# Kernel optimization log

Hardware: AMD Instinct MI355X
Metric: run time of the kernel (lower is better)

## Reference

```python
import jax, jax.numpy as jnp
import numpy as np

H = 2048          # hidden_size
I = 1024          # moe_intermediate_size
E = 32            # n_routed_experts
K = 4             # num_experts_per_tok
N_SHARED = 1
EPS = 1e-6


def setup_inputs() -> dict:
    key = jax.random.key(0)
    ks = jax.random.split(key, 8)
    s = 1.0 / np.sqrt(H)
    si = 1.0 / np.sqrt(I)
    return {
        "hidden_states": jax.random.normal(ks[0], (1, 4096, H), jnp.float32),
        "norm_w": jnp.ones((H,), jnp.float32),
        "gate_w": jax.random.normal(ks[1], (E, H), jnp.float32) * s,      # MoEGate.weight
        "w13": jax.random.normal(ks[2], (E, H, 2 * I), jnp.float32) * s,  # fused w1w3
        "w2": jax.random.normal(ks[3], (E, I, H), jnp.float32) * si,      # fused w2
        "shared_gate_w": jax.random.normal(ks[4], (H, I * N_SHARED), jnp.float32) * s,
        "shared_up_w": jax.random.normal(ks[5], (H, I * N_SHARED), jnp.float32) * s,
        "shared_down_w": jax.random.normal(ks[6], (I * N_SHARED, H), jnp.float32) * si,
    }


def _rmsnorm(x, w, eps=EPS):
    var = jnp.mean(jnp.square(x), axis=-1, keepdims=True)
    return x * jax.lax.rsqrt(var + eps) * w


def _moe_core(x, gate_w, w13, w2):
    # x: [T, H] (post-norm tokens)
    T = x.shape[0]
    N = T * K
    C = 2 * N // E

    # --- gate (fp32, F.linear) ---
    logits = jnp.einsum("th,eh->te", x.astype(jnp.float32), gate_w.astype(jnp.float32))
    scores = jax.nn.softmax(logits, axis=-1)
    topk_w, topk_ids = jax.lax.top_k(scores, K)           # [T, K]
    topk_w = topk_w / jnp.sum(topk_w, axis=-1, keepdims=True)  # norm_topk_prob

    # --- dispatch: sort token-expert pairs by expert ---
    flat_ids = topk_ids.reshape(-1)                        # [N] int
    flat_w = topk_w.reshape(-1)                            # [N]
    order = jnp.argsort(flat_ids)                          # stable sort by expert
    sorted_eid = flat_ids[order]                           # [N]
    tok = order // K                                       # source token per sorted slot
    counts = jnp.zeros((E,), jnp.int32).at[flat_ids].add(1)  # tokens_per_expert
    starts = jnp.cumsum(counts) - counts
    pos = jnp.arange(N) - starts[sorted_eid]               # position within expert group

    # scatter tokens into [E, C, H] buffer (OOB rows dropped; C sized so this ~never happens)
    buf = jnp.zeros((E, C, x.shape[1]), x.dtype).at[sorted_eid, pos].set(x[tok], mode="drop")

    # --- grouped expert FFN (swiglu) ---
    gu = jnp.einsum("ech,ehf->ecf", buf, w13)              # [E, C, 2I]
    g, u = jnp.split(gu, 2, axis=-1)
    act = jax.nn.silu(g) * u                               # swiglu
    eo = jnp.einsum("eci,eih->ech", act, w2)               # [E, C, H]

    # --- combine: gather back and weighted scatter-add per source token ---
    out_slots = eo[sorted_eid, pos]                        # [N, H]
    routed = jnp.zeros_like(x).at[tok].add(out_slots * flat_w[order][:, None])
    return routed


def reference(hidden_states, norm_w, gate_w, w13, w2, shared_gate_w, shared_up_w, shared_down_w):
    B, S, Hd = hidden_states.shape
    residual = hidden_states
    h = _rmsnorm(hidden_states, norm_w)                    # post_attention_layernorm
    x = h.reshape(-1, Hd)                                  # [T, H]

    routed = _moe_core(x, gate_w, w13, w2)                 # routed experts output

    # shared experts MLP (swiglu)
    shared = (jax.nn.silu(x @ shared_gate_w) * (x @ shared_up_w)) @ shared_down_w

    out = residual + (routed + shared).reshape(B, S, Hd)
    return out
```

## Files before the change

### kernel.cpp

```cpp
#include <hip/hip_runtime.h>
#include <hip/hip_bf16.h>
#include <math.h>

#define HD 2048
#define ID 1024
#define NE 32
#define TOPK 4
#define NTOK 4096
#define NSLOT (NTOK*TOPK)

typedef __attribute__((ext_vector_type(4))) float f32x4;
typedef __attribute__((ext_vector_type(8))) short bf16x8;
typedef unsigned short u16;
typedef unsigned int u32;

union U32x4BF { uint4 u; bf16x8 h; };

static __device__ __forceinline__ u16 f2bf(float f) {
  union { float f; u32 u; } v; v.f = f;
  u32 r = v.u + 0x7fffu + ((v.u >> 16) & 1u);
  return (u16)(r >> 16);
}

static __device__ __forceinline__ u32 cvtpk(float lo, float hi) {
  u32 r;
  asm("v_cvt_pk_bf16_f32 %0, %1, %2" : "=v"(r) : "v"(lo), "v"(hi));
  return r;
}

static __device__ __forceinline__ void barrier_lgkm() {
  asm volatile("s_waitcnt lgkmcnt(0)" ::: "memory");
  __builtin_amdgcn_s_barrier();
}

static __device__ __forceinline__ void loadBreg(const float* __restrict__ bg,
                                                const float* __restrict__ bu,
                                                u32 o0, u32 o1, u32 o2, u32 o3,
                                                u32 ldb, float bs[4][8]) {
  #pragma unroll
  for (int j = 0; j < 8; ++j) {
    bs[0][j] = bg[o0 + j*ldb];
    bs[1][j] = bu[o1 + j*ldb];
    bs[2][j] = bg[o2 + j*ldb];
    bs[3][j] = bu[o3 + j*ldb];
  }
}

static __device__ __forceinline__ void cvtB(const float bs[4][8], bf16x8 bfr[4]) {
  #pragma unroll
  for (int fn = 0; fn < 4; ++fn) {
    U32x4BF ub;
    ub.u.x = cvtpk(bs[fn][0], bs[fn][1]);
    ub.u.y = cvtpk(bs[fn][2], bs[fn][3]);
    ub.u.z = cvtpk(bs[fn][4], bs[fn][5]);
    ub.u.w = cvtpk(bs[fn][6], bs[fn][7]);
    bfr[fn] = ub.h;
  }
}

__global__ __launch_bounds__(256) void k_rmsnorm(const float* __restrict__ x,
                                                 const float* __restrict__ w,
                                                 u16* __restrict__ xn,
                                                 float* __restrict__ out) {
  int t = blockIdx.x, tid = threadIdx.x;
  const float* row = x + (size_t)t * HD;
  float4 v0 = ((const float4*)row)[tid*2+0];
  float4 v1 = ((const float4*)row)[tid*2+1];
  float* orow = out + (size_t)t * HD;
  ((float4*)orow)[tid*2+0] = v0;
  ((float4*)orow)[tid*2+1] = v1;
  float ss = v0.x*v0.x+v0.y*v0.y+v0.z*v0.z+v0.w*v0.w
           + v1.x*v1.x+v1.y*v1.y+v1.z*v1.z+v1.w*v1.w;
  #pragma unroll
  for (int d=1; d<64; d<<=1) ss += __shfl_xor(ss, d);
  __shared__ float red[4];
  if ((tid&63)==0) red[tid>>6] = ss;
  __syncthreads();
  float rs = rsqrtf((red[0]+red[1]+red[2]+red[3]) * (1.0f/HD) + 1e-6f);
  const float* wp = w + tid*8;
  float a[8] = {v0.x,v0.y,v0.z,v0.w,v1.x,v1.y,v1.z,v1.w};
  uint4 o;
  o.x = (u32)f2bf(a[0]*rs*wp[0]) | ((u32)f2bf(a[1]*rs*wp[1])<<16);
  o.y = (u32)f2bf(a[2]*rs*wp[2]) | ((u32)f2bf(a[3]*rs*wp[3])<<16);
  o.z = (u32)f2bf(a[4]*rs*wp[4]) | ((u32)f2bf(a[5]*rs*wp[5])<<16);
  o.w = (u32)f2bf(a[6]*rs*wp[6]) | ((u32)f2bf(a[7]*rs*wp[7])<<16);
  ((uint4*)xn)[(size_t)t*(HD/8) + tid] = o;
}

__global__ __launch_bounds__(256) void k_gate(const float* __restrict__ x,
                                              const float* __restrict__ w,
                                              const float* __restrict__ gw,
                                              int* __restrict__ topk_id,
                                              float* __restrict__ topk_w,
                                              int* __restrict__ counts) {
  __shared__ float xs[HD];
  __shared__ float red[4];
  __shared__ float logits[NE];
  int t = blockIdx.x, tid = threadIdx.x;
  const float* row = x + (size_t)t*HD;
  float4 v0 = ((const float4*)row)[tid*2+0];
  float4 v1 = ((const float4*)row)[tid*2+1];
  float ss = v0.x*v0.x+v0.y*v0.y+v0.z*v0.z+v0.w*v0.w
           + v1.x*v1.x+v1.y*v1.y+v1.z*v1.z+v1.w*v1.w;
  #pragma unroll
  for (int d=1; d<64; d<<=1) ss += __shfl_xor(ss, d);
  if ((tid&63)==0) red[tid>>6] = ss;
  __syncthreads();
  float rs = 1.0f / sqrtf((red[0]+red[1]+red[2]+red[3]) * (1.0f/HD) + 1e-6f);
  const float* wp = w + tid*8;
  float a[8] = {v0.x,v0.y,v0.z,v0.w,v1.x,v1.y,v1.z,v1.w};
  #pragma unroll
  for (int j=0;j<8;++j) xs[tid*8+j] = a[j]*rs*wp[j];
  __syncthreads();
  int wave = tid>>6, lane = tid&63;
  for (int ei=0; ei<8; ++ei) {
    int e = wave*8 + ei;
    const float* g = gw + (size_t)e*HD;
    float s = 0.f;
    #pragma unroll
    for (int j=0;j<HD/64;++j) s += xs[lane + j*64] * g[lane + j*64];
    #pragma unroll
    for (int d=1; d<64; d<<=1) s += __shfl_xor(s, d);
    if (lane==0) logits[e] = s;
  }
  __syncthreads();
  if (tid==0) {
    float best[TOPK]; int bid[TOPK]; unsigned used = 0;
    for (int k2=0;k2<TOPK;++k2) {
      float bv = -1e30f; int bi = 0;
      for (int i2=0;i2<NE;++i2)
        if (!((used>>i2)&1u) && logits[i2] > bv) { bv = logits[i2]; bi = i2; }
      used |= 1u<<bi; best[k2] = bv; bid[k2] = bi;
    }
    float mx = best[0], sum = 0.f, wv[TOPK];
    for (int k2=0;k2<TOPK;++k2) { wv[k2] = expf(best[k2]-mx); sum += wv[k2]; }
    float inv = 1.f/sum;
    for (int k2=0;k2<TOPK;++k2) {
      topk_id[t*TOPK+k2] = bid[k2];
      topk_w[t*TOPK+k2] = wv[k2]*inv;
      atomicAdd(&counts[bid[k2]], 1);
    }
  }
}

__global__ void k_zero(int* counts, int* cursors) {
  int i = threadIdx.x;
  if (i < NE) { counts[i] = 0; cursors[i] = 0; }
}

__global__ void k_scan(const int* __restrict__ counts, int* __restrict__ starts) {
  if (threadIdx.x==0 && blockIdx.x==0) {
    int acc = 0;
    for (int e=0;e<NE;++e) { starts[e] = acc; acc += counts[e]; }
  }
}

__global__ __launch_bounds__(256) void k_dispatch(const int* __restrict__ topk_id,
                                                  const float* __restrict__ topk_w,
                                                  const int* __restrict__ starts,
                                                  int* __restrict__ cursors,
                                                  int* __restrict__ slot_tok,
                                                  float* __restrict__ slot_w) {
  int i = blockIdx.x*256 + threadIdx.x;
  int e = topk_id[i];
  int p = atomicAdd(&cursors[e], 1);
  int slot = starts[e] + p;
  slot_tok[slot] = i >> 2;
  slot_w[slot] = topk_w[i];
}

__global__ __launch_bounds__(256, 2) void k_gemm_up(
    const u16* __restrict__ A, const float* __restrict__ w13,
    const float* __restrict__ sgw, const float* __restrict__ suw,
    const int* __restrict__ counts, const int* __restrict__ starts,
    const int* __restrict__ slot_tok,
    u16* __restrict__ act, u16* __restrict__ sact) {
  __shared__ u16 Al[2][4096];
  __shared__ int rowL[128];
  int t = threadIdx.x;
  int n0 = blockIdx.x * 128;
  int m0 = blockIdx.y * 128;
  int e  = blockIdx.z;
  bool routed = (e < NE);
  int M, rowbase;
  u16* actOut;
  if (routed) { M = counts[e]; rowbase = starts[e]; actOut = act; if (m0 >= M) return; }
  else { M = NTOK; rowbase = 0; actOut = sact; }
  if (t < 128) {
    int m = m0 + t;
    rowL[t] = routed ? slot_tok[rowbase + (m < M ? m : M-1)] : m;
  }
  __syncthreads();
  int r0i = t>>2;
  int segA = ((t&3) ^ ((r0i>>1)&3)) << 3;
  const u16* srcA0 = A + (size_t)rowL[r0i]*HD + segA;
  const u16* srcA1 = A + (size_t)rowL[r0i+64]*HD + segA;

  int lane = t&63, wn = t>>6;
  int l15 = lane&15, l4 = lane>>4;
  int aoffb = l15*32 + ((l4 ^ ((l15>>1)&3))<<3);

  const float *bbg, *bbu;
  u32 ldb, o0, o1, o2, o3;
  {
    int c0 = n0 + (wn*2+0)*16 + l15;
    int c1 = n0 + (wn*2+1)*16 + l15;
    if (routed) {
      ldb = 2*ID;
      bbg = w13 + (size_t)e*HD*2*ID; bbu = bbg;
      u32 rb = (u32)(l4*8)*ldb;
      o0 = rb + c0; o1 = rb + c0 + ID; o2 = rb + c1; o3 = rb + c1 + ID;
    } else {
      ldb = ID;
      bbg = sgw; bbu = suw;
      u32 rb = (u32)(l4*8)*ldb;
      o0 = rb + c0; o1 = rb + c0; o2 = rb + c1; o3 = rb + c1;
    }
  }
  u32 kadv = 32*ldb;

  f32x4 acc[8][4];
  #pragma unroll
  for (int fm=0;fm<8;++fm)
    #pragma unroll
    for (int fn=0;fn<4;++fn)
      acc[fm][fn] = (f32x4){0.f,0.f,0.f,0.f};

  uint4 aA0 = *(const uint4*)srcA0, aA1 = *(const uint4*)srcA1;
  srcA0 += 32; srcA1 += 32;
  float bsA[4][8]; loadBreg(bbg, bbu, o0,o1,o2,o3, ldb, bsA);
  o0 += kadv; o1 += kadv; o2 += kadv; o3 += kadv;
  uint4 aB0 = *(const uint4*)srcA0, aB1 = *(const uint4*)srcA1;
  srcA0 += 32; srcA1 += 32;
  float bsB[4][8]; loadBreg(bbg, bbu, o0,o1,o2,o3, ldb, bsB);
  o0 += kadv; o1 += kadv; o2 += kadv; o3 += kadv;
  *(uint4*)&Al[0][t*8] = aA0;
  *(uint4*)&Al[0][2048 + t*8] = aA1;
  barrier_lgkm();

  const int kiter = HD/32;
  for (int kt = 0; kt < kiter; kt += 2) {
    {
      bool pf = (kt+2 < kiter);
      if (pf) { aA0 = *(const uint4*)srcA0; aA1 = *(const uint4*)srcA1; srcA0 += 32; srcA1 += 32; }
      bf16x8 bfr[4]; cvtB(bsA, bfr);
      if (pf) { loadBreg(bbg, bbu, o0,o1,o2,o3, ldb, bsA);
                o0 += kadv; o1 += kadv; o2 += kadv; o3 += kadv; }
      __builtin_amdgcn_s_setprio(1);
      #pragma unroll
      for (int fm=0; fm<8; ++fm) {
        bf16x8 af = *(const bf16x8*)&Al[0][aoffb + fm*512];
        #pragma unroll
        for (int fn=0; fn<4; ++fn)
          acc[fm][fn] = __builtin_amdgcn_mfma_f32_16x16x32_bf16(af, bfr[fn], acc[fm][fn], 0,0,0);
      }
      __builtin_amdgcn_s_setprio(0);
      *(uint4*)&Al[1][t*8] = aB0;
      *(uint4*)&Al[1][2048 + t*8] = aB1;
      barrier_lgkm();
    }
    {
      bool pf = (kt+3 < kiter);
      if (pf) { aB0 = *(const uint4*)srcA0; aB1 = *(const uint4*)srcA1; srcA0 += 32; srcA1 += 32; }
      bf16x8 bfr[4]; cvtB(bsB, bfr);
      if (pf) { loadBreg(bbg, bbu, o0,o1,o2,o3, ldb, bsB);
                o0 += kadv; o1 += kadv; o2 += kadv; o3 += kadv; }
      __builtin_amdgcn_s_setprio(1);
      #pragma unroll
      for (int fm=0; fm<8; ++fm) {
        bf16x8 af = *(const bf16x8*)&Al[1][aoffb + fm*512];
        #pragma unroll
        for (int fn=0; fn<4; ++fn)
          acc[fm][fn] = __builtin_amdgcn_mfma_f32_16x16x32_bf16(af, bfr[fn], acc[fm][fn], 0,0,0);
      }
      __builtin_amdgcn_s_setprio(0);
      if (kt+2 < kiter) {
        *(uint4*)&Al[0][t*8] = aA0;
        *(uint4*)&Al[0][2048 + t*8] = aA1;
      }
      barrier_lgkm();
    }
  }
  #pragma unroll
  for (int fm=0; fm<8; ++fm) {
    #pragma unroll
    for (int fq=0; fq<2; ++fq) {
      f32x4 g = acc[fm][2*fq], u = acc[fm][2*fq+1];
      int col = n0 + (wn*2+fq)*16 + l15;
      #pragma unroll
      for (int r=0;r<4;++r) {
        int mloc = fm*16 + l4*4 + r;
        int m = m0 + mloc;
        if (m < M) {
          float gv = g[r];
          float av = gv / (1.f + expf(-gv)) * u[r];
          actOut[(size_t)(rowbase+m)*ID + col] = f2bf(av);
        }
      }
    }
  }
}

__global__ __launch_bounds__(256, 2) void k_gemm_down(
    const u16* __restrict__ act, const u16* __restrict__ sact,
    const float* __restrict__ w2, const float* __restrict__ sdw,
    const int* __restrict__ counts, const int* __restrict__ starts,
    const int* __restrict__ slot_tok, const float* __restrict__ slot_w,
    float* __restrict__ out) {
  __shared__ u16 Al[2][4096];
  __shared__ int tokL[128];
  __shared__ float wL[128];
  int t = threadIdx.x;
  int n0 = blockIdx.x * 256;
  int m0 = blockIdx.y * 128;
  int e  = blockIdx.z;
  bool routed = (e < NE);
  int M, rowbase;
  const u16* A;
  if (routed) { M = counts[e]; rowbase = starts[e]; A = act; if (m0 >= M) return; }
  else { M = NTOK; rowbase = 0; A = sact; }
  if (routed && t < 128) {
    int m = m0 + t;
    tokL[t] = (m<M) ? slot_tok[rowbase+m] : 0;
    wL[t]   = (m<M) ? slot_w[rowbase+m]  : 0.f;
  }
  if (routed) __syncthreads();
  int r0i = t>>2;
  int segA = ((t&3) ^ ((r0i>>1)&3)) << 3;
  int am0 = m0 + r0i, am1 = m0 + r0i + 64;
  const u16* srcA0 = A + (size_t)(rowbase + (am0 < M ? am0 : M-1))*ID + segA;
  const u16* srcA1 = A + (size_t)(rowbase + (am1 < M ? am1 : M-1))*ID + segA;

  int lane = t&63, wn = t>>6;
  int l15 = lane&15, l4 = lane>>4;
  int aoffb = l15*32 + ((l4 ^ ((l15>>1)&3))<<3);

  const float* bb = routed ? (w2 + (size_t)e*ID*HD) : sdw;
  const u32 ldb = HD;
  u32 rb = (u32)(l4*8)*ldb;
  u32 o0 = rb + n0 + wn*64 + 0*16 + l15;
  u32 o1 = rb + n0 + wn*64 + 1*16 + l15;
  u32 o2 = rb + n0 + wn*64 + 2*16 + l15;
  u32 o3 = rb + n0 + wn*64 + 3*16 + l15;
  const u32 kadv = 32*ldb;

  f32x4 acc[8][4];
  #pragma unroll
  for (int fm=0;fm<8;++fm)
    #pragma unroll
    for (int fn=0;fn<4;++fn)
      acc[fm][fn] = (f32x4){0.f,0.f,0.f,0.f};

  uint4 aA0 = *(const uint4*)srcA0, aA1 = *(const uint4*)srcA1;
  srcA0 += 32; srcA1 += 32;
  float bsA[4][8]; loadBreg(bb, bb, o0,o1,o2,o3, ldb, bsA);
  o0 += kadv; o1 += kadv; o2 += kadv; o3 += kadv;
  uint4 aB0 = *(const uint4*)srcA0, aB1 = *(const uint4*)srcA1;
  srcA0 += 32; srcA1 += 32;
  float bsB[4][8]; loadBreg(bb, bb, o0,o1,o2,o3, ldb, bsB);
  o0 += kadv; o1 += kadv; o2 += kadv; o3 += kadv;
  *(uint4*)&Al[0][t*8] = aA0;
  *(uint4*)&Al[0][2048 + t*8] = aA1;
  barrier_lgkm();

  const int kiter = ID/32;
  for (int kt = 0; kt < kiter; kt += 2) {
    {
      bool pf = (kt+2 < kiter);
      if (pf) { aA0 = *(const uint4*)srcA0; aA1 = *(const uint4*)srcA1; srcA0 += 32; srcA1 += 32; }
      bf16x8 bfr[4]; cvtB(bsA, bfr);
      if (pf) { loadBreg(bb, bb, o0,o1,o2,o3, ldb, bsA);
                o0 += kadv; o1 += kadv; o2 += kadv; o3 += kadv; }
      __builtin_amdgcn_s_setprio(1);
      #pragma unroll
      for (int fm=0; fm<8; ++fm) {
        bf16x8 af = *(const bf16x8*)&Al[0][aoffb + fm*512];
        #pragma unroll
        for (int fn=0; fn<4; ++fn)
          acc[fm][fn] = __builtin_amdgcn_mfma_f32_16x16x32_bf16(af, bfr[fn], acc[fm][fn], 0,0,0);
      }
      __builtin_amdgcn_s_setprio(0);
      *(uint4*)&Al[1][t*8] = aB0;
      *(uint4*)&Al[1][2048 + t*8] = aB1;
      barrier_lgkm();
    }
    {
      bool pf = (kt+3 < kiter);
      if (pf) { aB0 = *(const uint4*)srcA0; aB1 = *(const uint4*)srcA1; srcA0 += 32; srcA1 += 32; }
      bf16x8 bfr[4]; cvtB(bsB, bfr);
      if (pf) { loadBreg(bb, bb, o0,o1,o2,o3, ldb, bsB);
                o0 += kadv; o1 += kadv; o2 += kadv; o3 += kadv; }
      __builtin_amdgcn_s_setprio(1);
      #pragma unroll
      for (int fm=0; fm<8; ++fm) {
        bf16x8 af = *(const bf16x8*)&Al[1][aoffb + fm*512];
        #pragma unroll
        for (int fn=0; fn<4; ++fn)
          acc[fm][fn] = __builtin_amdgcn_mfma_f32_16x16x32_bf16(af, bfr[fn], acc[fm][fn], 0,0,0);
      }
      __builtin_amdgcn_s_setprio(0);
      if (kt+2 < kiter) {
        *(uint4*)&Al[0][t*8] = aA0;
        *(uint4*)&Al[0][2048 + t*8] = aA1;
      }
      barrier_lgkm();
    }
  }
  #pragma unroll
  for (int fm=0; fm<8; ++fm) {
    #pragma unroll
    for (int fn=0; fn<4; ++fn) {
      f32x4 v = acc[fm][fn];
      int col = n0 + wn*64 + fn*16 + l15;
      #pragma unroll
      for (int r=0;r<4;++r) {
        int mloc = fm*16 + l4*4 + r;
        int m = m0 + mloc;
        if (m < M) {
          if (routed) {
            atomicAdd(&out[(size_t)tokL[mloc]*HD + col], v[r]*wL[mloc]);
          } else {
            atomicAdd(&out[(size_t)m*HD + col], v[r]);
          }
        }
      }
    }
  }
}

extern "C" void kernel_launch(void* const* d_in, const int* in_sizes, int n_in,
                              void* d_out, int out_size, void* d_ws, size_t ws_size,
                              hipStream_t stream) {
  const float* x    = (const float*)d_in[0];
  const float* nw   = (const float*)d_in[1];
  const float* gw   = (const float*)d_in[2];
  const float* w13  = (const float*)d_in[3];
  const float* w2   = (const float*)d_in[4];
  const float* sgw  = (const float*)d_in[5];
  const float* suw  = (const float*)d_in[6];
  const float* sdw  = (const float*)d_in[7];
  float* out = (float*)d_out;

  char* p = (char*)d_ws;
  u16* xn   = (u16*)p;  p += (size_t)NTOK*HD*2;
  u16* act  = (u16*)p;  p += (size_t)NSLOT*ID*2;
  u16* sact = (u16*)p;  p += (size_t)NTOK*ID*2;
  int*   topk_id  = (int*)p;   p += (size_t)NTOK*TOPK*4;
  float* topk_w   = (float*)p; p += (size_t)NTOK*TOPK*4;
  int*   slot_tok = (int*)p;   p += (size_t)NSLOT*4;
  float* slot_w   = (float*)p; p += (size_t)NSLOT*4;
  int*   counts   = (int*)p;   p += 64*4;
  int*   cursors  = (int*)p;   p += 64*4;
  int*   starts   = (int*)p;   p += 64*4;

  k_zero<<<1, 64, 0, stream>>>(counts, cursors);
  k_rmsnorm<<<NTOK, 256, 0, stream>>>(x, nw, xn, out);
  k_gate<<<NTOK, 256, 0, stream>>>(x, nw, gw, topk_id, topk_w, counts);
  k_scan<<<1, 1, 0, stream>>>(counts, starts);
  k_dispatch<<<NSLOT/256, 256, 0, stream>>>(topk_id, topk_w, starts, cursors, slot_tok, slot_w);

  k_gemm_up<<<dim3(ID/128, 32, NE+1), 256, 0, stream>>>(
      xn, w13, sgw, suw, counts, starts, slot_tok, act, sact);
  k_gemm_down<<<dim3(HD/256, 32, NE+1), 256, 0, stream>>>(
      act, sact, w2, sdw, counts, starts, slot_tok, slot_w, out);
}
```

Before: 752.9 us.

## Fuse rmsnorm into gate kernel and retile GEMMs to 2x2 wave grid

Merges the rmsnorm and gate kernels into one prep kernel, so the input rows are read once and one launch goes away. Both grouped GEMMs move from a 1x4 wave layout to a 2x2 layout with half the N tile per block. This halves the per-wave accumulators, which allows the occupancy hint to rise from 2 to 3 blocks. The cost is that each block reloads the fp32 weight tiles over twice as many blocks, adding redundant global traffic and bf16 conversion work.

New measurement: 1.239 ms. 1.65x slower.

```diff
diff --git a/kernel.cpp b/kernel.cpp
--- a/kernel.cpp
+++ b/kernel.cpp
@@ -35,14 +35,14 @@
 
 static __device__ __forceinline__ void loadBreg(const float* __restrict__ bg,
                                                 const float* __restrict__ bu,
-                                                u32 o0, u32 o1, u32 o2, u32 o3,
-                                                u32 ldb, float bs[4][8]) {
+                                                const u32 o[4], u32 ldb,
+                                                float bs[4][8]) {
   #pragma unroll
   for (int j = 0; j < 8; ++j) {
-    bs[0][j] = bg[o0 + j*ldb];
-    bs[1][j] = bu[o1 + j*ldb];
-    bs[2][j] = bg[o2 + j*ldb];
-    bs[3][j] = bu[o3 + j*ldb];
+    bs[0][j] = bg[o[0] + j*ldb];
+    bs[1][j] = bu[o[1] + j*ldb];
+    bs[2][j] = bg[o[2] + j*ldb];
+    bs[3][j] = bu[o[3] + j*ldb];
   }
 }
 
@@ -58,38 +58,11 @@
   }
 }
 
-__global__ __launch_bounds__(256) void k_rmsnorm(const float* __restrict__ x,
-                                                 const float* __restrict__ w,
-                                                 u16* __restrict__ xn,
-                                                 float* __restrict__ out) {
-  int t = blockIdx.x, tid = threadIdx.x;
-  const float* row = x + (size_t)t * HD;
-  float4 v0 = ((const float4*)row)[tid*2+0];
-  float4 v1 = ((const float4*)row)[tid*2+1];
-  float* orow = out + (size_t)t * HD;
-  ((float4*)orow)[tid*2+0] = v0;
-  ((float4*)orow)[tid*2+1] = v1;
-  float ss = v0.x*v0.x+v0.y*v0.y+v0.z*v0.z+v0.w*v0.w
-           + v1.x*v1.x+v1.y*v1.y+v1.z*v1.z+v1.w*v1.w;
-  #pragma unroll
-  for (int d=1; d<64; d<<=1) ss += __shfl_xor(ss, d);
-  __shared__ float red[4];
-  if ((tid&63)==0) red[tid>>6] = ss;
-  __syncthreads();
-  float rs = rsqrtf((red[0]+red[1]+red[2]+red[3]) * (1.0f/HD) + 1e-6f);
-  const float* wp = w + tid*8;
-  float a[8] = {v0.x,v0.y,v0.z,v0.w,v1.x,v1.y,v1.z,v1.w};
-  uint4 o;
-  o.x = (u32)f2bf(a[0]*rs*wp[0]) | ((u32)f2bf(a[1]*rs*wp[1])<<16);
-  o.y = (u32)f2bf(a[2]*rs*wp[2]) | ((u32)f2bf(a[3]*rs*wp[3])<<16);
-  o.z = (u32)f2bf(a[4]*rs*wp[4]) | ((u32)f2bf(a[5]*rs*wp[5])<<16);
-  o.w = (u32)f2bf(a[6]*rs*wp[6]) | ((u32)f2bf(a[7]*rs*wp[7])<<16);
-  ((uint4*)xn)[(size_t)t*(HD/8) + tid] = o;
-}
-
-__global__ __launch_bounds__(256) void k_gate(const float* __restrict__ x,
+__global__ __launch_bounds__(256) void k_prep(const float* __restrict__ x,
                                               const float* __restrict__ w,
                                               const float* __restrict__ gw,
+                                              u16* __restrict__ xn,
+                                              float* __restrict__ out,
                                               int* __restrict__ topk_id,
                                               float* __restrict__ topk_w,
                                               int* __restrict__ counts) {
@@ -100,17 +73,27 @@
   const float* row = x + (size_t)t*HD;
   float4 v0 = ((const float4*)row)[tid*2+0];
   float4 v1 = ((const float4*)row)[tid*2+1];
+  float* orow = out + (size_t)t * HD;
+  ((float4*)orow)[tid*2+0] = v0;
+  ((float4*)orow)[tid*2+1] = v1;
   float ss = v0.x*v0.x+v0.y*v0.y+v0.z*v0.z+v0.w*v0.w
            + v1.x*v1.x+v1.y*v1.y+v1.z*v1.z+v1.w*v1.w;
   #pragma unroll
   for (int d=1; d<64; d<<=1) ss += __shfl_xor(ss, d);
   if ((tid&63)==0) red[tid>>6] = ss;
   __syncthreads();
-  float rs = 1.0f / sqrtf((red[0]+red[1]+red[2]+red[3]) * (1.0f/HD) + 1e-6f);
+  float rs = rsqrtf((red[0]+red[1]+red[2]+red[3]) * (1.0f/HD) + 1e-6f);
   const float* wp = w + tid*8;
   float a[8] = {v0.x,v0.y,v0.z,v0.w,v1.x,v1.y,v1.z,v1.w};
-  #pragma unroll
-  for (int j=0;j<8;++j) xs[tid*8+j] = a[j]*rs*wp[j];
+  float nv[8];
+  #pragma unroll
+  for (int j=0;j<8;++j) { nv[j] = a[j]*rs*wp[j]; xs[tid*8+j] = nv[j]; }
+  uint4 o;
+  o.x = (u32)f2bf(nv[0]) | ((u32)f2bf(nv[1])<<16);
+  o.y = (u32)f2bf(nv[2]) | ((u32)f2bf(nv[3])<<16);
+  o.z = (u32)f2bf(nv[4]) | ((u32)f2bf(nv[5])<<16);
+  o.w = (u32)f2bf(nv[6]) | ((u32)f2bf(nv[7])<<16);
+  ((uint4*)xn)[(size_t)t*(HD/8) + tid] = o;
   __syncthreads();
   int wave = tid>>6, lane = tid&63;
   for (int ei=0; ei<8; ++ei) {
@@ -169,7 +152,7 @@
   slot_w[slot] = topk_w[i];
 }
 
-__global__ __launch_bounds__(256, 2) void k_gemm_up(
+__global__ __launch_bounds__(256, 3) void k_gemm_up(
     const u16* __restrict__ A, const float* __restrict__ w13,
     const float* __restrict__ sgw, const float* __restrict__ suw,
     const int* __restrict__ counts, const int* __restrict__ starts,
@@ -178,7 +161,7 @@
   __shared__ u16 Al[2][4096];
   __shared__ int rowL[128];
   int t = threadIdx.x;
-  int n0 = blockIdx.x * 128;
+  int n0 = blockIdx.x * 64;
   int m0 = blockIdx.y * 128;
   int e  = blockIdx.z;
   bool routed = (e < NE);
@@ -196,44 +179,51 @@
   const u16* srcA0 = A + (size_t)rowL[r0i]*HD + segA;
   const u16* srcA1 = A + (size_t)rowL[r0i+64]*HD + segA;
 
-  int lane = t&63, wn = t>>6;
+  int lane = t&63, wave = t>>6, wr = wave>>1, wc = wave&1;
   int l15 = lane&15, l4 = lane>>4;
-  int aoffb = l15*32 + ((l4 ^ ((l15>>1)&3))<<3);
+  int aoff[4];
+  #pragma unroll
+  for (int f=0; f<4; ++f) {
+    int r = wr*64 + f*16 + l15;
+    aoff[f] = r*32 + ((l4 ^ ((r>>1)&3))<<3);
+  }
 
   const float *bbg, *bbu;
-  u32 ldb, o0, o1, o2, o3;
+  u32 ldb, o[4];
   {
-    int c0 = n0 + (wn*2+0)*16 + l15;
-    int c1 = n0 + (wn*2+1)*16 + l15;
+    int c0 = n0 + (wc*2+0)*16 + l15;
+    int c1 = n0 + (wc*2+1)*16 + l15;
     if (routed) {
       ldb = 2*ID;
       bbg = w13 + (size_t)e*HD*2*ID; bbu = bbg;
       u32 rb = (u32)(l4*8)*ldb;
-      o0 = rb + c0; o1 = rb + c0 + ID; o2 = rb + c1; o3 = rb + c1 + ID;
+      o[0] = rb + c0; o[1] = rb + c0 + ID; o[2] = rb + c1; o[3] = rb + c1 + ID;
     } else {
       ldb = ID;
       bbg = sgw; bbu = suw;
       u32 rb = (u32)(l4*8)*ldb;
-      o0 = rb + c0; o1 = rb + c0; o2 = rb + c1; o3 = rb + c1;
+      o[0] = rb + c0; o[1] = rb + c0; o[2] = rb + c1; o[3] = rb + c1;
     }
   }
   u32 kadv = 32*ldb;
 
-  f32x4 acc[8][4];
-  #pragma unroll
-  for (int fm=0;fm<8;++fm)
+  f32x4 acc[4][4];
+  #pragma unroll
+  for (int fm=0;fm<4;++fm)
     #pragma unroll
     for (int fn=0;fn<4;++fn)
       acc[fm][fn] = (f32x4){0.f,0.f,0.f,0.f};
 
   uint4 aA0 = *(const uint4*)srcA0, aA1 = *(const uint4*)srcA1;
   srcA0 += 32; srcA1 += 32;
-  float bsA[4][8]; loadBreg(bbg, bbu, o0,o1,o2,o3, ldb, bsA);
-  o0 += kadv; o1 += kadv; o2 += kadv; o3 += kadv;
+  float bsA[4][8]; loadBreg(bbg, bbu, o, ldb, bsA);
+  #pragma unroll
+  for (int i=0;i<4;++i) o[i] += kadv;
   uint4 aB0 = *(const uint4*)srcA0, aB1 = *(const uint4*)srcA1;
   srcA0 += 32; srcA1 += 32;
-  float bsB[4][8]; loadBreg(bbg, bbu, o0,o1,o2,o3, ldb, bsB);
-  o0 += kadv; o1 += kadv; o2 += kadv; o3 += kadv;
+  float bsB[4][8]; loadBreg(bbg, bbu, o, ldb, bsB);
+  #pragma unroll
+  for (int i=0;i<4;++i) o[i] += kadv;
   *(uint4*)&Al[0][t*8] = aA0;
   *(uint4*)&Al[0][2048 + t*8] = aA1;
   barrier_lgkm();
@@ -244,12 +234,13 @@
       bool pf = (kt+2 < kiter);
       if (pf) { aA0 = *(const uint4*)srcA0; aA1 = *(const uint4*)srcA1; srcA0 += 32; srcA1 += 32; }
       bf16x8 bfr[4]; cvtB(bsA, bfr);
-      if (pf) { loadBreg(bbg, bbu, o0,o1,o2,o3, ldb, bsA);
-                o0 += kadv; o1 += kadv; o2 += kadv; o3 += kadv; }
+      if (pf) { loadBreg(bbg, bbu, o, ldb, bsA);
+                #pragma unroll
+                for (int i=0;i<4;++i) o[i] += kadv; }
       __builtin_amdgcn_s_setprio(1);
       #pragma unroll
-      for (int fm=0; fm<8; ++fm) {
-        bf16x8 af = *(const bf16x8*)&Al[0][aoffb + fm*512];
+      for (int fm=0; fm<4; ++fm) {
+        bf16x8 af = *(const bf16x8*)&Al[0][aoff[fm]];
         #pragma unroll
         for (int fn=0; fn<4; ++fn)
           acc[fm][fn] = __builtin_amdgcn_mfma_f32_16x16x32_bf16(af, bfr[fn], acc[fm][fn], 0,0,0);
@@ -263,12 +254,13 @@
       bool pf = (kt+3 < kiter);
       if (pf) { aB0 = *(const uint4*)srcA0; aB1 = *(const uint4*)srcA1; srcA0 += 32; srcA1 += 32; }
       bf16x8 bfr[4]; cvtB(bsB, bfr);
-      if (pf) { loadBreg(bbg, bbu, o0,o1,o2,o3, ldb, bsB);
-                o0 += kadv; o1 += kadv; o2 += kadv; o3 += kadv; }
+      if (pf) { loadBreg(bbg, bbu, o, ldb, bsB);
+                #pragma unroll
+                for (int i=0;i<4;++i) o[i] += kadv; }
       __builtin_amdgcn_s_setprio(1);
       #pragma unroll
-      for (int fm=0; fm<8; ++fm) {
-        bf16x8 af = *(const bf16x8*)&Al[1][aoffb + fm*512];
+      for (int fm=0; fm<4; ++fm) {
+        bf16x8 af = *(const bf16x8*)&Al[1][aoff[fm]];
         #pragma unroll
         for (int fn=0; fn<4; ++fn)
           acc[fm][fn] = __builtin_amdgcn_mfma_f32_16x16x32_bf16(af, bfr[fn], acc[fm][fn], 0,0,0);
@@ -282,14 +274,14 @@
     }
   }
   #pragma unroll
-  for (int fm=0; fm<8; ++fm) {
-    #pragma unroll
-    for (int fq=0; fq<2; ++fq) {
-      f32x4 g = acc[fm][2*fq], u = acc[fm][2*fq+1];
-      int col = n0 + (wn*2+fq)*16 + l15;
+  for (int fm=0; fm<4; ++fm) {
+    #pragma unroll
+    for (int q=0; q<2; ++q) {
+      f32x4 g = acc[fm][2*q], u = acc[fm][2*q+1];
+      int col = n0 + (wc*2+q)*16 + l15;
       #pragma unroll
       for (int r=0;r<4;++r) {
-        int mloc = fm*16 + l4*4 + r;
+        int mloc = wr*64 + fm*16 + l4*4 + r;
         int m = m0 + mloc;
         if (m < M) {
           float gv = g[r];
@@ -301,7 +293,7 @@
   }
 }
 
-__global__ __launch_bounds__(256, 2) void k_gemm_down(
+__global__ __launch_bounds__(256, 3) void k_gemm_down(
     const u16* __restrict__ act, const u16* __restrict__ sact,
     const float* __restrict__ w2, const float* __restrict__ sdw,
     const int* __restrict__ counts, const int* __restrict__ starts,
@@ -311,7 +303,7 @@
   __shared__ int tokL[128];
   __shared__ float wL[128];
   int t = threadIdx.x;
-  int n0 = blockIdx.x * 256;
+  int n0 = blockIdx.x * 128;
   int m0 = blockIdx.y * 128;
   int e  = blockIdx.z;
   bool routed = (e < NE);
@@ -331,34 +323,42 @@
   const u16* srcA0 = A + (size_t)(rowbase + (am0 < M ? am0 : M-1))*ID + segA;
   const u16* srcA1 = A + (size_t)(rowbase + (am1 < M ? am1 : M-1))*ID + segA;
 
-  int lane = t&63, wn = t>>6;
+  int lane = t&63, wave = t>>6, wr = wave>>1, wc = wave&1;
   int l15 = lane&15, l4 = lane>>4;
-  int aoffb = l15*32 + ((l4 ^ ((l15>>1)&3))<<3);
+  int aoff[4];
+  #pragma unroll
+  for (int f=0; f<4; ++f) {
+    int r = wr*64 + f*16 + l15;
+    aoff[f] = r*32 + ((l4 ^ ((r>>1)&3))<<3);
+  }
 
   const float* bb = routed ? (w2 + (size_t)e*ID*HD) : sdw;
   const u32 ldb = HD;
-  u32 rb = (u32)(l4*8)*ldb;
-  u32 o0 = rb + n0 + wn*64 + 0*16 + l15;
-  u32 o1 = rb + n0 + wn*64 + 1*16 + l15;
-  u32 o2 = rb + n0 + wn*64 + 2*16 + l15;
-  u32 o3 = rb + n0 + wn*64 + 3*16 + l15;
+  u32 o[4];
+  {
+    u32 rb = (u32)(l4*8)*ldb;
+    #pragma unroll
+    for (int fn=0; fn<4; ++fn) o[fn] = rb + n0 + wc*64 + fn*16 + l15;
+  }
   const u32 kadv = 32*ldb;
 
-  f32x4 acc[8][4];
-  #pragma unroll
-  for (int fm=0;fm<8;++fm)
+  f32x4 acc[4][4];
+  #pragma unroll
+  for (int fm=0;fm<4;++fm)
     #pragma unroll
     for (int fn=0;fn<4;++fn)
       acc[fm][fn] = (f32x4){0.f,0.f,0.f,0.f};
 
   uint4 aA0 = *(const uint4*)srcA0, aA1 = *(const uint4*)srcA1;
   srcA0 += 32; srcA1 += 32;
-  float bsA[4][8]; loadBreg(bb, bb, o0,o1,o2,o3, ldb, bsA);
-  o0 += kadv; o1 += kadv; o2 += kadv; o3 += kadv;
+  float bsA[4][8]; loadBreg(bb, bb, o, ldb, bsA);
+  #pragma unroll
+  for (int i=0;i<4;++i) o[i] += kadv;
   uint4 aB0 = *(const uint4*)srcA0, aB1 = *(const uint4*)srcA1;
   srcA0 += 32; srcA1 += 32;
-  float bsB[4][8]; loadBreg(bb, bb, o0,o1,o2,o3, ldb, bsB);
-  o0 += kadv; o1 += kadv; o2 += kadv; o3 += kadv;
+  float bsB[4][8]; loadBreg(bb, bb, o, ldb, bsB);
+  #pragma unroll
+  for (int i=0;i<4;++i) o[i] += kadv;
   *(uint4*)&Al[0][t*8] = aA0;
   *(uint4*)&Al[0][2048 + t*8] = aA1;
   barrier_lgkm();
@@ -369,12 +369,13 @@
       bool pf = (kt+2 < kiter);
       if (pf) { aA0 = *(const uint4*)srcA0; aA1 = *(const uint4*)srcA1; srcA0 += 32; srcA1 += 32; }
       bf16x8 bfr[4]; cvtB(bsA, bfr);
-      if (pf) { loadBreg(bb, bb, o0,o1,o2,o3, ldb, bsA);
-                o0 += kadv; o1 += kadv; o2 += kadv; o3 += kadv; }
+      if (pf) { loadBreg(bb, bb, o, ldb, bsA);
+                #pragma unroll
+                for (int i=0;i<4;++i) o[i] += kadv; }
       __builtin_amdgcn_s_setprio(1);
       #pragma unroll
-      for (int fm=0; fm<8; ++fm) {
-        bf16x8 af = *(const bf16x8*)&Al[0][aoffb + fm*512];
+      for (int fm=0; fm<4; ++fm) {
+        bf16x8 af = *(const bf16x8*)&Al[0][aoff[fm]];
         #pragma unroll
         for (int fn=0; fn<4; ++fn)
           acc[fm][fn] = __builtin_amdgcn_mfma_f32_16x16x32_bf16(af, bfr[fn], acc[fm][fn], 0,0,0);
@@ -388,12 +389,13 @@
       bool pf = (kt+3 < kiter);
       if (pf) { aB0 = *(const uint4*)srcA0; aB1 = *(const uint4*)srcA1; srcA0 += 32; srcA1 += 32; }
       bf16x8 bfr[4]; cvtB(bsB, bfr);
-      if (pf) { loadBreg(bb, bb, o0,o1,o2,o3, ldb, bsB);
-                o0 += kadv; o1 += kadv; o2 += kadv; o3 += kadv; }
+      if (pf) { loadBreg(bb, bb, o, ldb, bsB);
+                #pragma unroll
+                for (int i=0;i<4;++i) o[i] += kadv; }
       __builtin_amdgcn_s_setprio(1);
       #pragma unroll
-      for (int fm=0; fm<8; ++fm) {
-        bf16x8 af = *(const bf16x8*)&Al[1][aoffb + fm*512];
+      for (int fm=0; fm<4; ++fm) {
+        bf16x8 af = *(const bf16x8*)&Al[1][aoff[fm]];
         #pragma unroll
         for (int fn=0; fn<4; ++fn)
           acc[fm][fn] = __builtin_amdgcn_mfma_f32_16x16x32_bf16(af, bfr[fn], acc[fm][fn], 0,0,0);
@@ -407,14 +409,14 @@
     }
   }
   #pragma unroll
-  for (int fm=0; fm<8; ++fm) {
+  for (int fm=0; fm<4; ++fm) {
     #pragma unroll
     for (int fn=0; fn<4; ++fn) {
       f32x4 v = acc[fm][fn];
-      int col = n0 + wn*64 + fn*16 + l15;
+      int col = n0 + wc*64 + fn*16 + l15;
       #pragma unroll
       for (int r=0;r<4;++r) {
-        int mloc = fm*16 + l4*4 + r;
+        int mloc = wr*64 + fm*16 + l4*4 + r;
         int m = m0 + mloc;
         if (m < M) {
           if (routed) {
@@ -454,13 +456,12 @@
   int*   starts   = (int*)p;   p += 64*4;
 
   k_zero<<<1, 64, 0, stream>>>(counts, cursors);
-  k_rmsnorm<<<NTOK, 256, 0, stream>>>(x, nw, xn, out);
-  k_gate<<<NTOK, 256, 0, stream>>>(x, nw, gw, topk_id, topk_w, counts);
+  k_prep<<<NTOK, 256, 0, stream>>>(x, nw, gw, xn, out, topk_id, topk_w, counts);
   k_scan<<<1, 1, 0, stream>>>(counts, starts);
   k_dispatch<<<NSLOT/256, 256, 0, stream>>>(topk_id, topk_w, starts, cursors, slot_tok, slot_w);
 
-  k_gemm_up<<<dim3(ID/128, 32, NE+1), 256, 0, stream>>>(
+  k_gemm_up<<<dim3(ID/64, 32, NE+1), 256, 0, stream>>>(
       xn, w13, sgw, suw, counts, starts, slot_tok, act, sact);
-  k_gemm_down<<<dim3(HD/256, 32, NE+1), 256, 0, stream>>>(
+  k_gemm_down<<<dim3(HD/128, 32, NE+1), 256, 0, stream>>>(
       act, sact, w2, sdw, counts, starts, slot_tok, slot_w, out);
 }
```

## Fuse rmsnorm into gate, replace atomic combine with slot buffer and XCD remap

Applied to the files above, without the earlier changes.

Merges the rmsnorm and gate kernels into one prep kernel so the input is read once. The down GEMM now writes per-slot results to a dense fp32 buffer and the shared expert adds into the output with plain stores. A new combine kernel then gathers each token's four slots and applies the routing weights. This replaces the scattered fp32 atomics with regular loads and stores, at the cost of a 128 MB intermediate buffer and an extra kernel pass. Block indices are also remapped so neighbouring tiles land on the same XCD, for better L2 reuse.

Result: slower. 1.210 ms (+60.7%).

```diff
diff --git a/kernel.cpp b/kernel.cpp
--- a/kernel.cpp
+++ b/kernel.cpp
@@ -31,6 +31,17 @@
 static __device__ __forceinline__ void barrier_lgkm() {
   asm volatile("s_waitcnt lgkmcnt(0)" ::: "memory");
   __builtin_amdgcn_s_barrier();
+}
+
+static __device__ __forceinline__ void xcd_remap(int bx, int by, int bz,
+                                                 int& x_, int& y_, int& z_) {
+  int lin = bx + 8*(by + 32*bz);
+  int xcd = lin & 7, s = lin >> 3;
+  x_ = s & 7;
+  int gg = s >> 3;
+  int gid = xcd + 8*gg;
+  y_ = gid & 31;
+  z_ = gid >> 5;
 }
 
 static __device__ __forceinline__ void loadBreg(const float* __restrict__ bg,
@@ -58,38 +69,11 @@
   }
 }
 
-__global__ __launch_bounds__(256) void k_rmsnorm(const float* __restrict__ x,
-                                                 const float* __restrict__ w,
-                                                 u16* __restrict__ xn,
-                                                 float* __restrict__ out) {
-  int t = blockIdx.x, tid = threadIdx.x;
-  const float* row = x + (size_t)t * HD;
-  float4 v0 = ((const float4*)row)[tid*2+0];
-  float4 v1 = ((const float4*)row)[tid*2+1];
-  float* orow = out + (size_t)t * HD;
-  ((float4*)orow)[tid*2+0] = v0;
-  ((float4*)orow)[tid*2+1] = v1;
-  float ss = v0.x*v0.x+v0.y*v0.y+v0.z*v0.z+v0.w*v0.w
-           + v1.x*v1.x+v1.y*v1.y+v1.z*v1.z+v1.w*v1.w;
-  #pragma unroll
-  for (int d=1; d<64; d<<=1) ss += __shfl_xor(ss, d);
-  __shared__ float red[4];
-  if ((tid&63)==0) red[tid>>6] = ss;
-  __syncthreads();
-  float rs = rsqrtf((red[0]+red[1]+red[2]+red[3]) * (1.0f/HD) + 1e-6f);
-  const float* wp = w + tid*8;
-  float a[8] = {v0.x,v0.y,v0.z,v0.w,v1.x,v1.y,v1.z,v1.w};
-  uint4 o;
-  o.x = (u32)f2bf(a[0]*rs*wp[0]) | ((u32)f2bf(a[1]*rs*wp[1])<<16);
-  o.y = (u32)f2bf(a[2]*rs*wp[2]) | ((u32)f2bf(a[3]*rs*wp[3])<<16);
-  o.z = (u32)f2bf(a[4]*rs*wp[4]) | ((u32)f2bf(a[5]*rs*wp[5])<<16);
-  o.w = (u32)f2bf(a[6]*rs*wp[6]) | ((u32)f2bf(a[7]*rs*wp[7])<<16);
-  ((uint4*)xn)[(size_t)t*(HD/8) + tid] = o;
-}
-
-__global__ __launch_bounds__(256) void k_gate(const float* __restrict__ x,
+__global__ __launch_bounds__(256) void k_prep(const float* __restrict__ x,
                                               const float* __restrict__ w,
                                               const float* __restrict__ gw,
+                                              u16* __restrict__ xn,
+                                              float* __restrict__ out,
                                               int* __restrict__ topk_id,
                                               float* __restrict__ topk_w,
                                               int* __restrict__ counts) {
@@ -100,17 +84,27 @@
   const float* row = x + (size_t)t*HD;
   float4 v0 = ((const float4*)row)[tid*2+0];
   float4 v1 = ((const float4*)row)[tid*2+1];
+  float* orow = out + (size_t)t * HD;
+  ((float4*)orow)[tid*2+0] = v0;
+  ((float4*)orow)[tid*2+1] = v1;
   float ss = v0.x*v0.x+v0.y*v0.y+v0.z*v0.z+v0.w*v0.w
            + v1.x*v1.x+v1.y*v1.y+v1.z*v1.z+v1.w*v1.w;
   #pragma unroll
   for (int d=1; d<64; d<<=1) ss += __shfl_xor(ss, d);
   if ((tid&63)==0) red[tid>>6] = ss;
   __syncthreads();
-  float rs = 1.0f / sqrtf((red[0]+red[1]+red[2]+red[3]) * (1.0f/HD) + 1e-6f);
+  float rs = rsqrtf((red[0]+red[1]+red[2]+red[3]) * (1.0f/HD) + 1e-6f);
   const float* wp = w + tid*8;
   float a[8] = {v0.x,v0.y,v0.z,v0.w,v1.x,v1.y,v1.z,v1.w};
-  #pragma unroll
-  for (int j=0;j<8;++j) xs[tid*8+j] = a[j]*rs*wp[j];
+  float nv[8];
+  #pragma unroll
+  for (int j=0;j<8;++j) { nv[j] = a[j]*rs*wp[j]; xs[tid*8+j] = nv[j]; }
+  uint4 o;
+  o.x = (u32)f2bf(nv[0]) | ((u32)f2bf(nv[1])<<16);
+  o.y = (u32)f2bf(nv[2]) | ((u32)f2bf(nv[3])<<16);
+  o.z = (u32)f2bf(nv[4]) | ((u32)f2bf(nv[5])<<16);
+  o.w = (u32)f2bf(nv[6]) | ((u32)f2bf(nv[7])<<16);
+  ((uint4*)xn)[(size_t)t*(HD/8) + tid] = o;
   __syncthreads();
   int wave = tid>>6, lane = tid&63;
   for (int ei=0; ei<8; ++ei) {
@@ -156,17 +150,16 @@
 }
 
 __global__ __launch_bounds__(256) void k_dispatch(const int* __restrict__ topk_id,
-                                                  const float* __restrict__ topk_w,
                                                   const int* __restrict__ starts,
                                                   int* __restrict__ cursors,
                                                   int* __restrict__ slot_tok,
-                                                  float* __restrict__ slot_w) {
+                                                  int* __restrict__ tok_slot) {
   int i = blockIdx.x*256 + threadIdx.x;
   int e = topk_id[i];
   int p = atomicAdd(&cursors[e], 1);
   int slot = starts[e] + p;
   slot_tok[slot] = i >> 2;
-  slot_w[slot] = topk_w[i];
+  tok_slot[i] = slot;
 }
 
 __global__ __launch_bounds__(256, 2) void k_gemm_up(
@@ -178,9 +171,11 @@
   __shared__ u16 Al[2][4096];
   __shared__ int rowL[128];
   int t = threadIdx.x;
-  int n0 = blockIdx.x * 128;
-  int m0 = blockIdx.y * 128;
-  int e  = blockIdx.z;
+  int bx, by, bz;
+  xcd_remap(blockIdx.x, blockIdx.y, blockIdx.z, bx, by, bz);
+  int n0 = bx * 128;
+  int m0 = by * 128;
+  int e  = bz;
   bool routed = (e < NE);
   int M, rowbase;
   u16* actOut;
@@ -305,26 +300,19 @@
     const u16* __restrict__ act, const u16* __restrict__ sact,
     const float* __restrict__ w2, const float* __restrict__ sdw,
     const int* __restrict__ counts, const int* __restrict__ starts,
-    const int* __restrict__ slot_tok, const float* __restrict__ slot_w,
-    float* __restrict__ out) {
+    float* __restrict__ dnbuf, float* __restrict__ out) {
   __shared__ u16 Al[2][4096];
-  __shared__ int tokL[128];
-  __shared__ float wL[128];
   int t = threadIdx.x;
-  int n0 = blockIdx.x * 256;
-  int m0 = blockIdx.y * 128;
-  int e  = blockIdx.z;
+  int bx, by, bz;
+  xcd_remap(blockIdx.x, blockIdx.y, blockIdx.z, bx, by, bz);
+  int n0 = bx * 256;
+  int m0 = by * 128;
+  int e  = bz;
   bool routed = (e < NE);
   int M, rowbase;
   const u16* A;
   if (routed) { M = counts[e]; rowbase = starts[e]; A = act; if (m0 >= M) return; }
   else { M = NTOK; rowbase = 0; A = sact; }
-  if (routed && t < 128) {
-    int m = m0 + t;
-    tokL[t] = (m<M) ? slot_tok[rowbase+m] : 0;
-    wL[t]   = (m<M) ? slot_w[rowbase+m]  : 0.f;
-  }
-  if (routed) __syncthreads();
   int r0i = t>>2;
   int segA = ((t&3) ^ ((r0i>>1)&3)) << 3;
   int am0 = m0 + r0i, am1 = m0 + r0i + 64;
@@ -418,13 +406,40 @@
         int m = m0 + mloc;
         if (m < M) {
           if (routed) {
-            atomicAdd(&out[(size_t)tokL[mloc]*HD + col], v[r]*wL[mloc]);
+            dnbuf[(size_t)(rowbase+m)*HD + col] = v[r];
           } else {
-            atomicAdd(&out[(size_t)m*HD + col], v[r]);
+            size_t oi = (size_t)m*HD + col;
+            out[oi] += v[r];
           }
         }
       }
     }
+  }
+}
+
+__global__ __launch_bounds__(256) void k_combine(
+    const float* __restrict__ dnbuf, const int* __restrict__ tok_slot,
+    const float* __restrict__ topk_w, float* __restrict__ out) {
+  int t = blockIdx.x, tid = threadIdx.x;
+  int s0 = tok_slot[t*TOPK+0], s1 = tok_slot[t*TOPK+1];
+  int s2 = tok_slot[t*TOPK+2], s3 = tok_slot[t*TOPK+3];
+  float w0 = topk_w[t*TOPK+0], w1 = topk_w[t*TOPK+1];
+  float w2 = topk_w[t*TOPK+2], w3 = topk_w[t*TOPK+3];
+  const float4* d0 = (const float4*)(dnbuf + (size_t)s0*HD);
+  const float4* d1 = (const float4*)(dnbuf + (size_t)s1*HD);
+  const float4* d2 = (const float4*)(dnbuf + (size_t)s2*HD);
+  const float4* d3 = (const float4*)(dnbuf + (size_t)s3*HD);
+  float4* op = (float4*)(out + (size_t)t*HD);
+  #pragma unroll
+  for (int h = 0; h < 2; ++h) {
+    int c = tid*2 + h;
+    float4 a = op[c];
+    float4 v0 = d0[c], v1 = d1[c], v2 = d2[c], v3 = d3[c];
+    a.x += w0*v0.x + w1*v1.x + w2*v2.x + w3*v3.x;
+    a.y += w0*v0.y + w1*v1.y + w2*v2.y + w3*v3.y;
+    a.z += w0*v0.z + w1*v1.z + w2*v2.z + w3*v3.z;
+    a.w += w0*v0.w + w1*v1.w + w2*v2.w + w3*v3.w;
+    op[c] = a;
   }
 }
 
@@ -442,25 +457,26 @@
   float* out = (float*)d_out;
 
   char* p = (char*)d_ws;
-  u16* xn   = (u16*)p;  p += (size_t)NTOK*HD*2;
-  u16* act  = (u16*)p;  p += (size_t)NSLOT*ID*2;
-  u16* sact = (u16*)p;  p += (size_t)NTOK*ID*2;
+  u16* xn      = (u16*)p;   p += (size_t)NTOK*HD*2;
+  u16* act     = (u16*)p;   p += (size_t)NSLOT*ID*2;
+  u16* sact    = (u16*)p;   p += (size_t)NTOK*ID*2;
+  float* dnbuf = (float*)p; p += (size_t)NSLOT*HD*4;
   int*   topk_id  = (int*)p;   p += (size_t)NTOK*TOPK*4;
   float* topk_w   = (float*)p; p += (size_t)NTOK*TOPK*4;
   int*   slot_tok = (int*)p;   p += (size_t)NSLOT*4;
-  float* slot_w   = (float*)p; p += (size_t)NSLOT*4;
+  int*   tok_slot = (int*)p;   p += (size_t)NSLOT*4;
   int*   counts   = (int*)p;   p += 64*4;
   int*   cursors  = (int*)p;   p += 64*4;
   int*   starts   = (int*)p;   p += 64*4;
 
   k_zero<<<1, 64, 0, stream>>>(counts, cursors);
-  k_rmsnorm<<<NTOK, 256, 0, stream>>>(x, nw, xn, out);
-  k_gate<<<NTOK, 256, 0, stream>>>(x, nw, gw, topk_id, topk_w, counts);
+  k_prep<<<NTOK, 256, 0, stream>>>(x, nw, gw, xn, out, topk_id, topk_w, counts);
   k_scan<<<1, 1, 0, stream>>>(counts, starts);
-  k_dispatch<<<NSLOT/256, 256, 0, stream>>>(topk_id, topk_w, starts, cursors, slot_tok, slot_w);
+  k_dispatch<<<NSLOT/256, 256, 0, stream>>>(topk_id, starts, cursors, slot_tok, tok_slot);
 
   k_gemm_up<<<dim3(ID/128, 32, NE+1), 256, 0, stream>>>(
       xn, w13, sgw, suw, counts, starts, slot_tok, act, sact);
   k_gemm_down<<<dim3(HD/256, 32, NE+1), 256, 0, stream>>>(
-      act, sact, w2, sdw, counts, starts, slot_tok, slot_w, out);
-}
+      act, sact, w2, sdw, counts, starts, dnbuf, out);
+  k_combine<<<NTOK, 256, 0, stream>>>(dnbuf, tok_slot, topk_w, out);
+}
```
